# Kernel optimization log

Hardware: AMD Instinct MI355X
Metric: run time of the kernel (lower is better)

## Reference

```python
import jax, jax.numpy as jnp
import numpy as np
import math

EMB = 512

def setup_inputs() -> dict:
    key = jax.random.key(0)
    ks = jax.random.split(key, 7)
    B, L, E = 4, 4096, EMB
    s = 1.0 / math.sqrt(E)
    return {
        "x": jax.random.normal(ks[0], (B, L, E), dtype=jnp.float32),
        "Wq": jax.random.normal(ks[1], (E, E), dtype=jnp.float32) * s,
        "bq": jax.random.normal(ks[2], (E,), dtype=jnp.float32) * 0.01,
        "Wk": jax.random.normal(ks[3], (E, E), dtype=jnp.float32) * s,
        "bk": jax.random.normal(ks[4], (E,), dtype=jnp.float32) * 0.01,
        "Wv": jax.random.normal(ks[5], (E, E), dtype=jnp.float32) * s,
        "bv": jax.random.normal(ks[6], (E,), dtype=jnp.float32) * 0.01,
    }

def reference(x, Wq, bq, Wk, bk, Wv, bv):
    # x: [B, L, E]; Linear weights stored torch-style [out, in]
    E = x.shape[-1]
    L = x.shape[1]
    q = jnp.einsum('ble,fe->blf', x, Wq) + bq
    k = jnp.einsum('ble,fe->blf', x, Wk) + bk
    v = jnp.einsum('ble,fe->blf', x, Wv) + bv
    qk = jnp.einsum('bqe,bke->bqk', q, k)  # [B, L, L]
    # causal mask: strict upper triangle filled with -1e9 BEFORE scaling (as in source)
    mask = jnp.triu(jnp.ones((L, L), dtype=bool), k=1)
    qk = jnp.where(mask, jnp.float32(-1e9), qk)
    att = jax.nn.softmax(qk / jnp.sqrt(jnp.float32(E)), axis=-1)
    return jnp.einsum('bqk,bke->bqe', att, v)
```

## Files before the change

### kernel.cpp

```cpp
#include <hip/hip_runtime.h>

typedef unsigned short u16;
typedef unsigned int u32;
typedef short bf16x8 __attribute__((ext_vector_type(8)));
typedef float f32x4 __attribute__((ext_vector_type(4)));
typedef u16 u16x8 __attribute__((ext_vector_type(8)));
typedef u16 u16x4 __attribute__((ext_vector_type(4)));

typedef const __attribute__((address_space(1))) u32* gas_ptr;
typedef __attribute__((address_space(3))) u32* las_ptr;

#define LQ   4096
#define EMB  512
#define NB   4
#define MROWS (NB * LQ)
#define QSCALE 0.04419417382415922f

__device__ __forceinline__ u16 f2bf(float f) {
  unsigned u = __builtin_bit_cast(unsigned, f);
  u += 0x7fffu + ((u >> 16) & 1u);
  return (u16)(u >> 16);
}
__device__ __forceinline__ float bf2f(u16 h) {
  unsigned u = ((unsigned)h) << 16;
  return __builtin_bit_cast(float, u);
}

__global__ void prep_w(const float* __restrict__ Wq, const float* __restrict__ bq,
                       const float* __restrict__ Wk, const float* __restrict__ bk,
                       const float* __restrict__ Wv, const float* __restrict__ bv,
                       u16* __restrict__ wqb, u16* __restrict__ wkb, u16* __restrict__ wvb,
                       float* __restrict__ bias) {
  int i = blockIdx.x * 256 + threadIdx.x;
  if (i < EMB * EMB) {
    wqb[i] = f2bf(Wq[i] * QSCALE);
    wkb[i] = f2bf(Wk[i]);
    wvb[i] = f2bf(Wv[i]);
  }
  if (i < EMB) {
    bias[i]           = bq[i] * QSCALE;
    bias[EMB + i]     = bk[i];
    bias[2 * EMB + i] = bv[i];
  }
}

__global__ void prep_x(const float* __restrict__ x, u16* __restrict__ xb) {
  int i = blockIdx.x * 256 + threadIdx.x;
  const float4* p = (const float4*)(x + (size_t)i * 8);
  float4 a = p[0], b = p[1];
  u16x8 o;
  o[0] = f2bf(a.x); o[1] = f2bf(a.y); o[2] = f2bf(a.z); o[3] = f2bf(a.w);
  o[4] = f2bf(b.x); o[5] = f2bf(b.y); o[6] = f2bf(b.z); o[7] = f2bf(b.w);
  *(u16x8*)(xb + (size_t)i * 8) = o;
}

__device__ __forceinline__ void stage128_256t(const u16* g, int ld, u16* lds, int tid) {
  int wave = tid >> 6;
#pragma unroll
  for (int p = 0; p < 4; ++p) {
    int c = tid + p * 256;
    int row = c >> 3, hh = c & 7;
    int h = hh ^ (row & 7);
    const u16* src = g + (size_t)row * ld + h * 8;
    u16* dst = lds + wave * 512 + p * 2048;
    __builtin_amdgcn_global_load_lds((gas_ptr)(const void*)src, (las_ptr)(void*)dst, 16, 0, 0);
  }
}

__device__ __forceinline__ void gemm_core_db(
    const u16* __restrict__ A, int lda,
    const u16* __restrict__ B, int ldb,
    int kIters, u16* lds,
    f32x4 acc[4][4], int tid, int lane, int wr, int wc)
{
  stage128_256t(A, lda, lds, tid);
  stage128_256t(B, ldb, lds + 8192, tid);
  for (int kb = 0; kb < kIters; ++kb) {
    u16* ldsA = lds + (kb & 1) * 16384;
    u16* ldsB = ldsA + 8192;
    __syncthreads();
    if (kb + 1 < kIters) {
      u16* nA = lds + ((kb + 1) & 1) * 16384;
      stage128_256t(A + (kb + 1) * 64, lda, nA, tid);
      stage128_256t(B + (kb + 1) * 64, ldb, nA + 8192, tid);
    }
#pragma unroll
    for (int s = 0; s < 2; ++s) {
      bf16x8 af[4], bfr[4];
#pragma unroll
      for (int m = 0; m < 4; ++m) {
        int row = wr * 64 + m * 16 + (lane & 15);
        int hh = (s * 4 + (lane >> 4)) ^ (row & 7);
        af[m] = *(const bf16x8*)(ldsA + row * 64 + hh * 8);
      }
#pragma unroll
      for (int n = 0; n < 4; ++n) {
        int row = wc * 64 + n * 16 + (lane & 15);
        int hh = (s * 4 + (lane >> 4)) ^ (row & 7);
        bfr[n] = *(const bf16x8*)(ldsB + row * 64 + hh * 8);
      }
#pragma unroll
      for (int m = 0; m < 4; ++m)
#pragma unroll
        for (int n = 0; n < 4; ++n)
          acc[m][n] = __builtin_amdgcn_mfma_f32_16x16x32_bf16(af[m], bfr[n], acc[m][n], 0, 0, 0);
    }
  }
}

__global__ __launch_bounds__(256, 2) void k_qkv(
    const u16* __restrict__ xb,
    const u16* __restrict__ w0, const u16* __restrict__ w1, const u16* __restrict__ w2,
    const float* __restrict__ bias,
    u16* __restrict__ o0, u16* __restrict__ o1, u16* __restrict__ o2)
{
  __shared__ __align__(16) u16 lds[32768];
  int bi = blockIdx.x;
  int which = bi >> 9;
  int t = bi & 511;
  int rt = t >> 2, ct = t & 3;
  const u16* W = (which == 0) ? w0 : (which == 1) ? w1 : w2;
  const float* bs = bias + which * EMB;
  int tid = threadIdx.x, lane = tid & 63, wave = tid >> 6;
  int wr = wave >> 1, wc = wave & 1;
  f32x4 acc[4][4];
#pragma unroll
  for (int m = 0; m < 4; ++m)
#pragma unroll
    for (int n = 0; n < 4; ++n) acc[m][n] = (f32x4)0.0f;

  gemm_core_db(xb + (size_t)rt * 128 * EMB, EMB,
               W + (size_t)ct * 128 * EMB, EMB, EMB / 64,
               lds, acc, tid, lane, wr, wc);

#pragma unroll
  for (int m = 0; m < 4; ++m)
#pragma unroll
    for (int n = 0; n < 4; ++n) {
      int row0 = rt * 128 + wr * 64 + m * 16 + ((lane >> 4) << 2);
      int col  = ct * 128 + wc * 64 + n * 16 + (lane & 15);
      float bv = bs[col];
      if (which < 2) {
        u16* out = (which == 0) ? o0 : o1;
#pragma unroll
        for (int r = 0; r < 4; ++r)
          out[(size_t)(row0 + r) * EMB + col] = f2bf(acc[m][n][r] + bv);
      } else {
        int b = row0 >> 12, l0 = row0 & (LQ - 1);
        u16x4 pk;
#pragma unroll
        for (int r = 0; r < 4; ++r) pk[r] = f2bf(acc[m][n][r] + bv);
        *(u16x4*)(o2 + ((size_t)(b * EMB + col)) * LQ + l0) = pk;
      }
    }
}

__global__ __launch_bounds__(256, 2) void k_qk(
    const u16* __restrict__ Q, const u16* __restrict__ K,
    u16* __restrict__ S, int bstart)
{
  __shared__ __align__(16) u16 lds[32768];
  int t = blockIdx.x;
  int b_local = t / 528;
  int i = t - b_local * 528;
  int qi = (int)((sqrtf(8.f * (float)i + 1.f) - 1.f) * 0.5f);
  while ((qi + 1) * (qi + 2) / 2 <= i) ++qi;
  while (qi * (qi + 1) / 2 > i) --qi;
  int ki = i - qi * (qi + 1) / 2;
  int bg = bstart + b_local;

  int tid = threadIdx.x, lane = tid & 63, wave = tid >> 6;
  int wr = wave >> 1, wc = wave & 1;
  f32x4 acc[4][4];
#pragma unroll
  for (int m = 0; m < 4; ++m)
#pragma unroll
    for (int n = 0; n < 4; ++n) acc[m][n] = (f32x4)0.0f;

  gemm_core_db(Q + ((size_t)bg * LQ + qi * 128) * EMB, EMB,
               K + ((size_t)bg * LQ + ki * 128) * EMB, EMB, EMB / 64,
               lds, acc, tid, lane, wr, wc);

  u16* Sb = S + (size_t)b_local * LQ * LQ;
#pragma unroll
  for (int m = 0; m < 4; ++m)
#pragma unroll
    for (int n = 0; n < 4; ++n) {
      int row0 = qi * 128 + wr * 64 + m * 16 + ((lane >> 4) << 2);
      int col  = ki * 128 + wc * 64 + n * 16 + (lane & 15);
#pragma unroll
      for (int r = 0; r < 4; ++r) {
        int row = row0 + r;
        float v = (col > row) ? -1e9f : acc[m][n][r];
        Sb[(size_t)row * LQ + col] = f2bf(v);
      }
    }
}

__global__ __launch_bounds__(512, 2) void k_pv2(
    const u16* __restrict__ S, const u16* __restrict__ Vt,
    float* __restrict__ out, int bstart, int bcount)
{
  __shared__ __align__(16) u16 lds[49152];
  int bi = blockIdx.x;
  int per = 2 * bcount;
  int idx = bi / per;
  int rem = bi - idx * per;
  int rt = 31 - idx;
  int ct = rem / bcount;
  int b_local = rem - ct * bcount;
  int bg = bstart + b_local;
  int kIters = 2 * (rt + 1);

  const u16* Ap = S + ((size_t)b_local * LQ + rt * 128) * LQ;
  const u16* Bp = Vt + ((size_t)bg * EMB + ct * 256) * LQ;

  int tid = threadIdx.x, lane = tid & 63, wave = tid >> 6;
  int wr = wave >> 1, wc = wave & 1;
  int l15 = lane & 15, lhi = lane >> 4;

  f32x4 acc[2][8];
#pragma unroll
  for (int m = 0; m < 2; ++m)
#pragma unroll
    for (int n = 0; n < 8; ++n) acc[m][n] = (f32x4)0.0f;
  float mrun[2] = {-3.0e38f, -3.0e38f};
  float lrun[2] = {0.f, 0.f};

  {
#pragma unroll
    for (int p = 0; p < 2; ++p) {
      int c = tid + p * 512;
      int row = c >> 3, hh = c & 7;
      int h = hh ^ (row & 7);
      __builtin_amdgcn_global_load_lds((gas_ptr)(const void*)(Ap + (size_t)row * LQ + h * 8),
                                       (las_ptr)(void*)(lds + wave * 512 + p * 4096), 16, 0, 0);
    }
#pragma unroll
    for (int p = 0; p < 4; ++p) {
      int c = tid + p * 512;
      int row = c >> 3, hh = c & 7;
      int h = hh ^ (row & 7);
      __builtin_amdgcn_global_load_lds((gas_ptr)(const void*)(Bp + (size_t)row * LQ + h * 8),
                                       (las_ptr)(void*)(lds + 8192 + wave * 512 + p * 4096), 16, 0, 0);
    }
  }

  for (int kb = 0; kb < kIters; ++kb) {
    u16* ldsA = lds + (kb & 1) * 24576;
    u16* ldsB = ldsA + 8192;
    __syncthreads();
    if (kb + 1 < kIters) {
      u16* nA = lds + ((kb + 1) & 1) * 24576;
      const u16* ga = Ap + (kb + 1) * 64;
      const u16* gb = Bp + (kb + 1) * 64;
#pragma unroll
      for (int p = 0; p < 2; ++p) {
        int c = tid + p * 512;
        int row = c >> 3, hh = c & 7;
        int h = hh ^ (row & 7);
        __builtin_amdgcn_global_load_lds((gas_ptr)(const void*)(ga + (size_t)row * LQ + h * 8),
                                         (las_ptr)(void*)(nA + wave * 512 + p * 4096), 16, 0, 0);
      }
#pragma unroll
      for (int p = 0; p < 4; ++p) {
        int c = tid + p * 512;
        int row = c >> 3, hh = c & 7;
        int h = hh ^ (row & 7);
        __builtin_amdgcn_global_load_lds((gas_ptr)(const void*)(gb + (size_t)row * LQ + h * 8),
                                         (las_ptr)(void*)(nA + 8192 + wave * 512 + p * 4096), 16, 0, 0);
      }
    }

    float sv[2][16];
#pragma unroll
    for (int m = 0; m < 2; ++m) {
      int row = wr * 32 + m * 16 + l15;
#pragma unroll
      for (int s = 0; s < 2; ++s) {
        int hh = (s * 4 + lhi) ^ (row & 7);
        u16x8 raw = *(const u16x8*)(ldsA + row * 64 + hh * 8);
#pragma unroll
        for (int j = 0; j < 8; ++j) sv[m][s * 8 + j] = bf2f(raw[j]);
      }
    }
    float tmax[2];
#pragma unroll
    for (int m = 0; m < 2; ++m) {
      float tm = sv[m][0];
#pragma unroll
      for (int k = 1; k < 16; ++k) tm = fmaxf(tm, sv[m][k]);
      tm = fmaxf(tm, __shfl_xor(tm, 16));
      tm = fmaxf(tm, __shfl_xor(tm, 32));
      tmax[m] = tm;
    }
    bool need = (tmax[0] > mrun[0] + 8.f) || (tmax[1] > mrun[1] + 8.f);
    if (__any(need)) {
#pragma unroll
      for (int m = 0; m < 2; ++m) {
        float mn = fmaxf(mrun[m], tmax[m]);
        float f = __expf(mrun[m] - mn);
        mrun[m] = mn;
        lrun[m] *= f;
#pragma unroll
        for (int r = 0; r < 4; ++r) {
          float fr = __shfl(f, lhi * 4 + r);
#pragma unroll
          for (int n = 0; n < 8; ++n) acc[m][n][r] *= fr;
        }
      }
    }
    u16x8 pf[2][2];
#pragma unroll
    for (int m = 0; m < 2; ++m) {
      float ts = 0.f;
#pragma unroll
      for (int s = 0; s < 2; ++s)
#pragma unroll
        for (int j = 0; j < 8; ++j) {
          float p = __expf(sv[m][s * 8 + j] - mrun[m]);
          ts += p;
          pf[m][s][j] = f2bf(p);
        }
      ts += __shfl_xor(ts, 16);
      ts += __shfl_xor(ts, 32);
      lrun[m] += ts;
    }
#pragma unroll
    for (int s = 0; s < 2; ++s) {
#pragma unroll
      for (int n = 0; n < 8; ++n) {
        int col = wc * 128 + n * 16 + l15;
        int hh = (s * 4 + lhi) ^ (col & 7);
        bf16x8 bv = *(const bf16x8*)(ldsB + col * 64 + hh * 8);
#pragma unroll
        for (int m = 0; m < 2; ++m)
          acc[m][n] = __builtin_amdgcn_mfma_f32_16x16x32_bf16(
              __builtin_bit_cast(bf16x8, pf[m][s]), bv, acc[m][n], 0, 0, 0);
      }
    }
  }

#pragma unroll
  for (int m = 0; m < 2; ++m) {
    float linv = 1.0f / lrun[m];
#pragma unroll
    for (int r = 0; r < 4; ++r) {
      float fr = __shfl(linv, lhi * 4 + r);
      int grow = rt * 128 + wr * 32 + m * 16 + lhi * 4 + r;
#pragma unroll
      for (int n = 0; n < 8; ++n) {
        int col = ct * 256 + wc * 128 + n * 16 + l15;
        out[((size_t)bg * LQ + grow) * EMB + col] = acc[m][n][r] * fr;
      }
    }
  }
}

extern "C" void kernel_launch(void* const* d_in, const int* in_sizes, int n_in,
                              void* d_out, int out_size, void* d_ws, size_t ws_size,
                              hipStream_t stream) {
  const float* x  = (const float*)d_in[0];
  const float* Wq = (const float*)d_in[1];
  const float* bq = (const float*)d_in[2];
  const float* Wk = (const float*)d_in[3];
  const float* bk = (const float*)d_in[4];
  const float* Wv = (const float*)d_in[5];
  const float* bv = (const float*)d_in[6];

  char* ws = (char*)d_ws;
  size_t off = 0;
  u16* xb  = (u16*)(ws + off); off += (size_t)MROWS * EMB * 2;
  u16* wqb = (u16*)(ws + off); off += (size_t)EMB * EMB * 2;
  u16* wkb = (u16*)(ws + off); off += (size_t)EMB * EMB * 2;
  u16* wvb = (u16*)(ws + off); off += (size_t)EMB * EMB * 2;
  float* bias = (float*)(ws + off); off += 3 * EMB * 4;
  off = (off + 255) & ~(size_t)255;
  u16* Qb  = (u16*)(ws + off); off += (size_t)MROWS * EMB * 2;
  u16* Kb  = (u16*)(ws + off); off += (size_t)MROWS * EMB * 2;
  u16* Vtb = (u16*)(ws + off); off += (size_t)MROWS * EMB * 2;
  size_t fixed = off;
  size_t s_full = (size_t)NB * LQ * LQ * 2;
  int bcap = (ws_size >= fixed + s_full) ? NB : 1;
  u16* Sb = (u16*)(ws + fixed);

  prep_w<<<(EMB * EMB + 255) / 256, 256, 0, stream>>>(Wq, bq, Wk, bk, Wv, bv,
                                                      wqb, wkb, wvb, bias);
  prep_x<<<(MROWS * EMB / 8) / 256, 256, 0, stream>>>(x, xb);

  k_qkv<<<1536, 256, 0, stream>>>(xb, wqb, wkb, wvb, bias, Qb, Kb, Vtb);

  for (int bs = 0; bs < NB; bs += bcap) {
    int bc = (bs + bcap <= NB) ? bcap : (NB - bs);
    k_qk<<<528 * bc, 256, 0, stream>>>(Qb, Kb, Sb, bs);
    k_pv2<<<64 * bc, 512, 0, stream>>>(Sb, Vtb, (float*)d_out, bs, bc);
  }
}
```

Before: 257.2 us.

## Pair causal row tiles per block and narrow PV column tile

Each block of the P·V kernel now handles two row tiles (rtA and 31-rtA) one after the other, so every block does the same amount of causal work instead of 2 to 64 iterations. The output column tile shrinks from 256 to 128, which halves the accumulator registers and the LDS footprint, and launch bounds drop to one block per CU. The grid size stays the same. In exchange, each S tile is loaded and exponentiated by four column-tile blocks instead of two, doubling S memory traffic and softmax work.

```diff
diff --git a/kernel.cpp b/kernel.cpp
--- a/kernel.cpp
+++ b/kernel.cpp
@@ -197,80 +197,90 @@
     }
 }
 
-__global__ __launch_bounds__(512, 2) void k_pv2(
+__global__ __launch_bounds__(512, 1) void k_pv2(
     const u16* __restrict__ S, const u16* __restrict__ Vt,
     float* __restrict__ out, int bstart, int bcount)
 {
-  __shared__ __align__(16) u16 lds[49152];
+  __shared__ __align__(16) u16 lds[32768];
   int bi = blockIdx.x;
-  int per = 2 * bcount;
-  int idx = bi / per;
-  int rem = bi - idx * per;
-  int rt = 31 - idx;
+  int per = 4 * bcount;
+  int pairidx = bi / per;
+  int rem = bi - pairidx * per;
   int ct = rem / bcount;
   int b_local = rem - ct * bcount;
   int bg = bstart + b_local;
-  int kIters = 2 * (rt + 1);
-
-  const u16* Ap = S + ((size_t)b_local * LQ + rt * 128) * LQ;
-  const u16* Bp = Vt + ((size_t)bg * EMB + ct * 256) * LQ;
+
+  int rtA = pairidx, rtB = 31 - pairidx;
+  int unitsA = 2 * (rtA + 1);
+  int total = unitsA + 2 * (rtB + 1);
+
+  const u16* Sbase = S + (size_t)b_local * LQ * LQ;
+  const u16* Bp = Vt + ((size_t)bg * EMB + ct * 128) * LQ;
 
   int tid = threadIdx.x, lane = tid & 63, wave = tid >> 6;
-  int wr = wave >> 1, wc = wave & 1;
+  int wr = wave >> 2, wc = wave & 3;
+  wr = wave >> 1; wc = wave & 1;
   int l15 = lane & 15, lhi = lane >> 4;
 
-  f32x4 acc[2][8];
+  f32x4 acc[2][4];
 #pragma unroll
   for (int m = 0; m < 2; ++m)
 #pragma unroll
-    for (int n = 0; n < 8; ++n) acc[m][n] = (f32x4)0.0f;
+    for (int n = 0; n < 4; ++n) acc[m][n] = (f32x4)0.0f;
   float mrun[2] = {-3.0e38f, -3.0e38f};
   float lrun[2] = {0.f, 0.f};
 
-  {
+  auto stage_unit = [&](int i) {
+    int ph = (i >= unitsA);
+    int kb = ph ? (i - unitsA) : i;
+    int rt = ph ? rtB : rtA;
+    const u16* ga = Sbase + ((size_t)rt * 128) * LQ + kb * 64;
+    const u16* gb = Bp + kb * 64;
+    u16* buf = lds + (i & 1) * 16384;
 #pragma unroll
     for (int p = 0; p < 2; ++p) {
       int c = tid + p * 512;
       int row = c >> 3, hh = c & 7;
       int h = hh ^ (row & 7);
-      __builtin_amdgcn_global_load_lds((gas_ptr)(const void*)(Ap + (size_t)row * LQ + h * 8),
-                                       (las_ptr)(void*)(lds + wave * 512 + p * 4096), 16, 0, 0);
-    }
-#pragma unroll
-    for (int p = 0; p < 4; ++p) {
-      int c = tid + p * 512;
-      int row = c >> 3, hh = c & 7;
-      int h = hh ^ (row & 7);
-      __builtin_amdgcn_global_load_lds((gas_ptr)(const void*)(Bp + (size_t)row * LQ + h * 8),
-                                       (las_ptr)(void*)(lds + 8192 + wave * 512 + p * 4096), 16, 0, 0);
-    }
-  }
-
-  for (int kb = 0; kb < kIters; ++kb) {
-    u16* ldsA = lds + (kb & 1) * 24576;
+      __builtin_amdgcn_global_load_lds((gas_ptr)(const void*)(ga + (size_t)row * LQ + h * 8),
+                                       (las_ptr)(void*)(buf + wave * 512 + p * 4096), 16, 0, 0);
+      __builtin_amdgcn_global_load_lds((gas_ptr)(const void*)(gb + (size_t)row * LQ + h * 8),
+                                       (las_ptr)(void*)(buf + 8192 + wave * 512 + p * 4096), 16, 0, 0);
+    }
+  };
+
+  auto epilogue = [&](int rt) {
+#pragma unroll
+    for (int m = 0; m < 2; ++m) {
+      float linv = 1.0f / lrun[m];
+#pragma unroll
+      for (int r = 0; r < 4; ++r) {
+        float fr = __shfl(linv, lhi * 4 + r);
+        int grow = rt * 128 + wr * 32 + m * 16 + lhi * 4 + r;
+#pragma unroll
+        for (int n = 0; n < 4; ++n) {
+          int col = ct * 128 + wc * 64 + n * 16 + l15;
+          out[((size_t)bg * LQ + grow) * EMB + col] = acc[m][n][r] * fr;
+        }
+      }
+    }
+#pragma unroll
+    for (int m = 0; m < 2; ++m) {
+#pragma unroll
+      for (int n = 0; n < 4; ++n) acc[m][n] = (f32x4)0.0f;
+      mrun[m] = -3.0e38f;
+      lrun[m] = 0.f;
+    }
+  };
+
+  stage_unit(0);
+
+  for (int i = 0; i < total; ++i) {
+    u16* ldsA = lds + (i & 1) * 16384;
     u16* ldsB = ldsA + 8192;
     __syncthreads();
-    if (kb + 1 < kIters) {
-      u16* nA = lds + ((kb + 1) & 1) * 24576;
-      const u16* ga = Ap + (kb + 1) * 64;
-      const u16* gb = Bp + (kb + 1) * 64;
-#pragma unroll
-      for (int p = 0; p < 2; ++p) {
-        int c = tid + p * 512;
-        int row = c >> 3, hh = c & 7;
-        int h = hh ^ (row & 7);
-        __builtin_amdgcn_global_load_lds((gas_ptr)(const void*)(ga + (size_t)row * LQ + h * 8),
-                                         (las_ptr)(void*)(nA + wave * 512 + p * 4096), 16, 0, 0);
-      }
-#pragma unroll
-      for (int p = 0; p < 4; ++p) {
-        int c = tid + p * 512;
-        int row = c >> 3, hh = c & 7;
-        int h = hh ^ (row & 7);
-        __builtin_amdgcn_global_load_lds((gas_ptr)(const void*)(gb + (size_t)row * LQ + h * 8),
-                                         (las_ptr)(void*)(nA + 8192 + wave * 512 + p * 4096), 16, 0, 0);
-      }
-    }
+    if (i + 1 < total) stage_unit(i + 1);
+    if (i == unitsA) epilogue(rtA);
 
     float sv[2][16];
 #pragma unroll
@@ -306,7 +316,7 @@
         for (int r = 0; r < 4; ++r) {
           float fr = __shfl(f, lhi * 4 + r);
 #pragma unroll
-          for (int n = 0; n < 8; ++n) acc[m][n][r] *= fr;
+          for (int n = 0; n < 4; ++n) acc[m][n][r] *= fr;
         }
       }
     }
@@ -329,8 +339,8 @@
 #pragma unroll
     for (int s = 0; s < 2; ++s) {
 #pragma unroll
-      for (int n = 0; n < 8; ++n) {
-        int col = wc * 128 + n * 16 + l15;
+      for (int n = 0; n < 4; ++n) {
+        int col = wc * 64 + n * 16 + l15;
         int hh = (s * 4 + lhi) ^ (col & 7);
         bf16x8 bv = *(const bf16x8*)(ldsB + col * 64 + hh * 8);
 #pragma unroll
@@ -340,21 +350,7 @@
       }
     }
   }
-
-#pragma unroll
-  for (int m = 0; m < 2; ++m) {
-    float linv = 1.0f / lrun[m];
-#pragma unroll
-    for (int r = 0; r < 4; ++r) {
-      float fr = __shfl(linv, lhi * 4 + r);
-      int grow = rt * 128 + wr * 32 + m * 16 + lhi * 4 + r;
-#pragma unroll
-      for (int n = 0; n < 8; ++n) {
-        int col = ct * 256 + wc * 128 + n * 16 + l15;
-        out[((size_t)bg * LQ + grow) * EMB + col] = acc[m][n][r] * fr;
-      }
-    }
-  }
+  epilogue(rtB);
 }
 
 extern "C" void kernel_launch(void* const* d_in, const int* in_sizes, int n_in,
```

Measured after the change: 244.7 us. -4.8%, faster.
